# Kernel optimization log

Hardware: AMD Instinct MI355X
Metric: run time of the kernel (lower is better)

Reference implementation:

```python
import jax, jax.numpy as jnp
import numpy as np

B, S, D, H, DH = 2, 2048, 768, 12, 64
GAMMA = 0.5
SMOOTHING = 1.0  # softmax_attn_smoothing scalar (non-trainable weight in the original)
SCALE = 1.0 / float(np.sqrt(DH))


def setup_inputs() -> dict:
    key = jax.random.key(0)
    ks = jax.random.split(key, 8)
    w = 0.02
    return {
        "inp": jax.random.normal(ks[0], (B, S, D), dtype=jnp.float32),
        "pos_emb": jax.random.normal(ks[1], (S, D), dtype=jnp.float32),
        "Wq_inp": jax.random.normal(ks[2], (D, H * DH), dtype=jnp.float32) * w,
        "Wk_inp": jax.random.normal(ks[3], (D, H * DH), dtype=jnp.float32) * w,
        "Wq_pos": jax.random.normal(ks[4], (D, H * DH), dtype=jnp.float32) * w,
        "Wk_pos": jax.random.normal(ks[5], (D, H * DH), dtype=jnp.float32) * w,
        "Wv": jax.random.normal(ks[6], (D, H * DH), dtype=jnp.float32) * w,
        "Wo": jax.random.normal(ks[7], (H * DH, D), dtype=jnp.float32) * w,
    }


def reference(inp, pos_emb, Wq_inp, Wk_inp, Wq_pos, Wk_pos, Wv, Wo):
    # projections; note original reshape order: [..., d_head, n_head]
    q_i = (inp @ Wq_inp).reshape(B, S, DH, H)
    k_i = (inp @ Wk_inp).reshape(B, S, DH, H)
    q_p = (pos_emb @ Wq_pos).reshape(S, DH, H)
    k_p = (pos_emb @ Wk_pos).reshape(S, DH, H)
    v = (inp @ Wv).reshape(B, S, DH, H)

    # content-content stream: [B,S,S,H], softmax over key axis (axis=2)
    score_inp = jnp.einsum("bidh,bjdh->bijh", q_i, k_i) * (SCALE * SMOOTHING)
    prob_inp = jax.nn.softmax(score_inp, axis=2)

    # position-position stream: [S,S,H], softmax over key axis (axis=1)
    score_pos = jnp.einsum("idh,jdh->ijh", q_p, k_p) * (SCALE * SMOOTHING)
    prob_pos = jax.nn.softmax(score_pos, axis=1)[None]  # [1,S,S,H]

    # gamma blend of the two attention distributions
    attn_prob = (1.0 - GAMMA) * prob_inp + GAMMA * prob_pos  # [B,S,S,H]

    # V-weighted sum, merge heads as [..., h, d] per the original 'bihd' output
    attn_out = jnp.einsum("bijh,bjdh->bihd", attn_prob, v).reshape(B, S, H * DH)
    attn_out = attn_out @ Wo  # [B,S,D]
    return attn_out, attn_prob
```

## Files before the change

kernel.cpp:

```cpp
#include <hip/hip_runtime.h>
#include <hip/hip_bf16.h>

constexpr int NH  = 12;
constexpr int SEQ = 2048;
constexpr int DHD = 64;
constexpr int DIM = 768;
constexpr float QSCALE = 0.125f * 1.44269504088896f;

typedef __bf16 bf16x8 __attribute__((ext_vector_type(8)));
typedef __bf16 bf16x4 __attribute__((ext_vector_type(4)));
typedef float  f32x4  __attribute__((ext_vector_type(4)));

#define MFMA16(a, b, c) __builtin_amdgcn_mfma_f32_16x16x32_bf16((a), (b), (c), 0, 0, 0)

__global__ __launch_bounds__(256) void conv_kernel(
    const float* __restrict__ inp, const float* __restrict__ pos,
    __bf16* __restrict__ Ab, __bf16* __restrict__ Pb)
{
    const int idx = blockIdx.x * 256 + threadIdx.x;
    constexpr int N8I = 4096 * 768 / 8;
    constexpr int N8P = 2048 * 768 / 8;
    if (idx >= N8I + N8P) return;
    const float* src; __bf16* dst; int off;
    if (idx < N8I) { src = inp; dst = Ab; off = idx; }
    else           { src = pos; dst = Pb; off = idx - N8I; }
    const float4 v0 = *reinterpret_cast<const float4*>(&src[(size_t)off * 8]);
    const float4 v1 = *reinterpret_cast<const float4*>(&src[(size_t)off * 8 + 4]);
    bf16x8 t;
    t[0] = (__bf16)v0.x; t[1] = (__bf16)v0.y; t[2] = (__bf16)v0.z; t[3] = (__bf16)v0.w;
    t[4] = (__bf16)v1.x; t[5] = (__bf16)v1.y; t[6] = (__bf16)v1.z; t[7] = (__bf16)v1.w;
    *reinterpret_cast<bf16x8*>(&dst[(size_t)off * 8]) = t;
}

__global__ __launch_bounds__(256) void packw_kernel(
    const float* __restrict__ Wqi, const float* __restrict__ Wki,
    const float* __restrict__ Wvv, const float* __restrict__ Wqp,
    const float* __restrict__ Wkp, __bf16* __restrict__ Wp)
{
    const int kt = blockIdx.x, h = blockIdx.y, z = blockIdx.z;
    const int k0 = kt * 64;
    const float* W; float scale = 1.0f;
    if (z == 0)      { W = Wqi; scale = QSCALE; }
    else if (z == 1) { W = Wki; }
    else if (z == 2) { W = Wvv; }
    else if (z == 3) { W = Wqp; scale = QSCALE; }
    else             { W = Wkp; }

    __shared__ __bf16 lds[64][68];
    const int tid = threadIdx.x;
    {
        const int d = tid & 63, kq = tid >> 6;
        #pragma unroll
        for (int rep = 0; rep < 16; ++rep) {
            const int kk = rep * 4 + kq;
            lds[kk][d] = (__bf16)(W[(size_t)(k0 + kk) * DIM + d * 12 + h] * scale);
        }
    }
    __syncthreads();
    {
        const int k = tid & 63, dq = tid >> 6;
        const size_t slab = ((size_t)z * 12 + h) * 64;
        #pragma unroll
        for (int rep = 0; rep < 16; ++rep) {
            const int d = rep * 4 + dq;
            Wp[(slab + d) * DIM + k0 + k] = lds[k][d];
        }
    }
}

__global__ __launch_bounds__(256) void proj_kernel(
    const __bf16* __restrict__ Ab, const __bf16* __restrict__ Pb,
    const __bf16* __restrict__ Wp,
    __bf16* __restrict__ Qi, __bf16* __restrict__ Ki, __bf16* __restrict__ Vsd,
    __bf16* __restrict__ Qp, __bf16* __restrict__ Kp)
{
    const int bx = blockIdx.x, h = blockIdx.y, z = blockIdx.z;
    if (z >= 3 && bx >= 8) return;
    const int tid = threadIdx.x, lane = tid & 63, wv = tid >> 6;
    const int l15 = lane & 15, lg = lane >> 4;
    const int m_w = bx * 256 + wv * 64;

    const __bf16* Asrc = (z < 3) ? Ab : Pb;
    const __bf16* Wsl = Wp + ((size_t)z * 12 + h) * 64 * DIM;

    f32x4 acc[4][4] = {};

    for (int kt = 0; kt < 24; ++kt) {
        const int k0 = kt * 32;
        bf16x8 a[4], b[4];
        #pragma unroll
        for (int mf = 0; mf < 4; ++mf)
            a[mf] = *reinterpret_cast<const bf16x8*>(
                &Asrc[(size_t)(m_w + mf * 16 + l15) * DIM + k0 + lg * 8]);
        #pragma unroll
        for (int nf = 0; nf < 4; ++nf)
            b[nf] = *reinterpret_cast<const bf16x8*>(
                &Wsl[(size_t)(nf * 16 + l15) * DIM + k0 + lg * 8]);
        #pragma unroll
        for (int mf = 0; mf < 4; ++mf)
            #pragma unroll
            for (int nf = 0; nf < 4; ++nf)
                acc[mf][nf] = MFMA16(a[mf], b[nf], acc[mf][nf]);
    }

    __bf16* outp = (z == 0) ? Qi : (z == 1) ? Ki : (z == 2) ? Vsd : (z == 3) ? Qp : Kp;
    #pragma unroll
    for (int mf = 0; mf < 4; ++mf)
        #pragma unroll
        for (int r = 0; r < 4; ++r) {
            const int m = m_w + mf * 16 + lg * 4 + r;
            const int s = m & 2047;
            const int slab = (z < 3) ? ((m >> 11) * 12 + h) : h;
            const size_t base = ((size_t)slab * SEQ + s) * DHD;
            #pragma unroll
            for (int nf = 0; nf < 4; ++nf)
                outp[base + nf * 16 + l15] = (__bf16)acc[mf][nf][r];
        }
}

__global__ __launch_bounds__(256) void vtrans_kernel(
    const __bf16* __restrict__ Vsd, __bf16* __restrict__ Vt)
{
    const int s0 = blockIdx.x * 64, slab = blockIdx.y;
    __shared__ __bf16 lds[64][66];
    const int tid = threadIdx.x;
    {
        const int rr = tid >> 3, cq = tid & 7;
        #pragma unroll
        for (int rep = 0; rep < 2; ++rep) {
            const int r2 = rr + rep * 32;
            *reinterpret_cast<bf16x8*>(&lds[r2][cq * 8]) =
                *reinterpret_cast<const bf16x8*>(
                    &Vsd[((size_t)slab * SEQ + s0 + r2) * DHD + cq * 8]);
        }
    }
    __syncthreads();
    {
        const int dd = tid >> 3, sq = tid & 7;
        #pragma unroll
        for (int rep = 0; rep < 2; ++rep) {
            const int d2 = dd + rep * 32;
            bf16x8 v;
            #pragma unroll
            for (int q = 0; q < 8; ++q) v[q] = lds[sq * 8 + q][d2];
            *reinterpret_cast<bf16x8*>(&Vt[((size_t)slab * DHD + d2) * SEQ + s0 + sq * 8]) = v;
        }
    }
}

__global__ __launch_bounds__(64) void stats_kernel(
    const __bf16* __restrict__ Qi, const __bf16* __restrict__ Ki,
    const __bf16* __restrict__ Qp, const __bf16* __restrict__ Kp,
    float* __restrict__ m_ws, float* __restrict__ l_ws)
{
    const int bx = blockIdx.x, h = blockIdx.y, bb = blockIdx.z;
    const int lane = threadIdx.x;
    const int l15 = lane & 15, lg = lane >> 4;
    const int i0 = bx * 16;

    const __bf16* Q = (bb < 2) ? Qi + ((size_t)bb * NH + h) * SEQ * DHD
                               : Qp + (size_t)h * SEQ * DHD;
    const __bf16* K = (bb < 2) ? Ki + ((size_t)bb * NH + h) * SEQ * DHD
                               : Kp + (size_t)h * SEQ * DHD;

    bf16x8 a[2];
    #pragma unroll
    for (int ks = 0; ks < 2; ++ks)
        a[ks] = *reinterpret_cast<const bf16x8*>(
            &Q[(size_t)(i0 + l15) * DHD + ks * 32 + lg * 8]);

    float mr[4], lr[4];
    #pragma unroll
    for (int r = 0; r < 4; ++r) { mr[r] = -1e30f; lr[r] = 0.0f; }

    for (int jt = 0; jt < 32; ++jt) {
        const int j0 = jt * 64;
        bf16x8 bk[2][4];
        #pragma unroll
        for (int ks = 0; ks < 2; ++ks)
            #pragma unroll
            for (int nf = 0; nf < 4; ++nf)
                bk[ks][nf] = *reinterpret_cast<const bf16x8*>(
                    &K[(size_t)(j0 + nf * 16 + l15) * DHD + ks * 32 + lg * 8]);
        f32x4 c[4] = {};
        #pragma unroll
        for (int ks = 0; ks < 2; ++ks)
            #pragma unroll
            for (int nf = 0; nf < 4; ++nf)
                c[nf] = MFMA16(a[ks], bk[ks][nf], c[nf]);

        #pragma unroll
        for (int r = 0; r < 4; ++r) {
            const float x01 = fmaxf(c[0][r], c[1][r]);
            const float x23 = fmaxf(c[2][r], c[3][r]);
            const float mn = fmaxf(mr[r], fmaxf(x01, x23));
            lr[r] = lr[r] * exp2f(mr[r] - mn)
                  + exp2f(c[0][r] - mn) + exp2f(c[1][r] - mn)
                  + exp2f(c[2][r] - mn) + exp2f(c[3][r] - mn);
            mr[r] = mn;
        }
    }

    #pragma unroll
    for (int msk = 1; msk < 16; msk <<= 1)
        #pragma unroll
        for (int r = 0; r < 4; ++r) {
            const float mo = __shfl_xor(mr[r], msk);
            const float lo = __shfl_xor(lr[r], msk);
            const float mn = fmaxf(mr[r], mo);
            lr[r] = lr[r] * exp2f(mr[r] - mn) + lo * exp2f(mo - mn);
            mr[r] = mn;
        }

    if (l15 == 0) {
        const size_t base = ((size_t)bb * NH + h) * SEQ + i0;
        #pragma unroll
        for (int r = 0; r < 4; ++r) {
            m_ws[base + lg * 4 + r] = mr[r];
            l_ws[base + lg * 4 + r] = lr[r];
        }
    }
}

__global__ __launch_bounds__(384) void emit_kernel(
    const __bf16* __restrict__ Qi, const __bf16* __restrict__ Ki,
    const __bf16* __restrict__ Qp, const __bf16* __restrict__ Kp,
    const __bf16* __restrict__ Vt,
    const float* __restrict__ m_ws, const float* __restrict__ l_ws,
    float* __restrict__ out1, float* __restrict__ attn_pre)
{
    const int it = blockIdx.x, js = blockIdx.y, b = blockIdx.z;
    const int i0 = it * 16;
    const int tid = threadIdx.x, lane = tid & 63, wv = tid >> 6;
    const int l15 = lane & 15, lg = lane >> 4;

    __shared__ __align__(16) __bf16 pbuf[2][12][16][40];
    __shared__ float ml[12][16][4];

    if (tid < 192) {
        const int h = tid >> 4, i = tid & 15;
        const size_t bi  = ((size_t)b * NH + h) * SEQ + i0 + i;
        const size_t ppi = ((size_t)2 * NH + h) * SEQ + i0 + i;
        ml[h][i][0] = m_ws[bi];
        ml[h][i][1] = 0.5f / l_ws[bi];
        ml[h][i][2] = m_ws[ppi];
        ml[h][i][3] = 0.5f / l_ws[ppi];
    }
    __syncthreads();

    const __bf16* Kb[2][2];
    bf16x8 aQ[2][2][2];
    #pragma unroll
    for (int hh = 0; hh < 2; ++hh) {
        const int h = wv * 2 + hh;
        Kb[hh][0] = Ki + ((size_t)b * NH + h) * SEQ * DHD;
        Kb[hh][1] = Kp + (size_t)h * SEQ * DHD;
        #pragma unroll
        for (int ks = 0; ks < 2; ++ks) {
            aQ[hh][0][ks] = *reinterpret_cast<const bf16x8*>(
                &Qi[(((size_t)b * NH + h) * SEQ + i0 + l15) * DHD + ks * 32 + lg * 8]);
            aQ[hh][1][ks] = *reinterpret_cast<const bf16x8*>(
                &Qp[((size_t)h * SEQ + i0 + l15) * DHD + ks * 32 + lg * 8]);
        }
    }

    bf16x8 kf[2][2][2][2];
    {
        const int j0 = js * 256;
        #pragma unroll
        for (int hh = 0; hh < 2; ++hh)
            #pragma unroll
            for (int st = 0; st < 2; ++st)
                #pragma unroll
                for (int nf = 0; nf < 2; ++nf)
                    #pragma unroll
                    for (int ks = 0; ks < 2; ++ks)
                        kf[hh][st][nf][ks] = *reinterpret_cast<const bf16x8*>(
                            &Kb[hh][st][(size_t)(j0 + nf * 16 + l15) * DHD + ks * 32 + lg * 8]);
    }

    f32x4 acc[2][4] = {};

    #pragma unroll 1
    for (int jt = 0; jt < 8; ++jt) {
        const int j0 = js * 256 + jt * 32;
        const int jn = (js * 256 + (jt + 1) * 32) & (SEQ - 1);
        const int buf = jt & 1;

        f32x4 ci[2][2] = {}, cq[2][2] = {};
        #pragma unroll
        for (int hh = 0; hh < 2; ++hh)
            #pragma unroll
            for (int ks = 0; ks < 2; ++ks)
                #pragma unroll
                for (int nf = 0; nf < 2; ++nf) {
                    ci[hh][nf] = MFMA16(aQ[hh][0][ks], kf[hh][0][nf][ks], ci[hh][nf]);
                    cq[hh][nf] = MFMA16(aQ[hh][1][ks], kf[hh][1][nf][ks], cq[hh][nf]);
                }

        #pragma unroll
        for (int hh = 0; hh < 2; ++hh)
            #pragma unroll
            for (int st = 0; st < 2; ++st)
                #pragma unroll
                for (int nf = 0; nf < 2; ++nf)
                    #pragma unroll
                    for (int ks = 0; ks < 2; ++ks)
                        kf[hh][st][nf][ks] = *reinterpret_cast<const bf16x8*>(
                            &Kb[hh][st][(size_t)(jn + nf * 16 + l15) * DHD + ks * 32 + lg * 8]);

        #pragma unroll
        for (int hh = 0; hh < 2; ++hh) {
            const int h = wv * 2 + hh;
            #pragma unroll
            for (int r = 0; r < 4; ++r) {
                const int i = lg * 4 + r;
                const f32x4 mlv = *reinterpret_cast<const f32x4*>(&ml[h][i][0]);
                #pragma unroll
                for (int nf = 0; nf < 2; ++nf) {
                    const float pi_ = exp2f(ci[hh][nf][r] - mlv[0]) * mlv[1];
                    const float pq_ = exp2f(cq[hh][nf][r] - mlv[2]) * mlv[3];
                    pbuf[buf][h][i][nf * 16 + l15] = (__bf16)(pi_ + pq_);
                }
            }
        }

        #pragma unroll
        for (int hh = 0; hh < 2; ++hh) {
            const int h = wv * 2 + hh;
            const bf16x8 ap = *reinterpret_cast<const bf16x8*>(&pbuf[buf][h][l15][lg * 8]);
            #pragma unroll
            for (int nf = 0; nf < 4; ++nf) {
                const bf16x8 bv = *reinterpret_cast<const bf16x8*>(
                    &Vt[(((size_t)b * NH + h) * DHD + nf * 16 + l15) * SEQ + j0 + lg * 8]);
                acc[hh][nf] = MFMA16(ap, bv, acc[hh][nf]);
            }
        }
        __syncthreads();

        for (int p = tid; p < 512; p += 384) {
            const int i = p >> 5, jj = p & 31;
            const size_t base = (((size_t)(b * SEQ + i0 + i)) * SEQ + j0 + jj) * 12;
            f32x4 v0, v1, v2;
            #pragma unroll
            for (int q = 0; q < 4; ++q) {
                v0[q] = (float)pbuf[buf][q][i][jj];
                v1[q] = (float)pbuf[buf][4 + q][i][jj];
                v2[q] = (float)pbuf[buf][8 + q][i][jj];
            }
            *reinterpret_cast<f32x4*>(&out1[base])     = v0;
            *reinterpret_cast<f32x4*>(&out1[base + 4]) = v1;
            *reinterpret_cast<f32x4*>(&out1[base + 8]) = v2;
        }
    }

    #pragma unroll
    for (int hh = 0; hh < 2; ++hh) {
        const int h = wv * 2 + hh;
        #pragma unroll
        for (int nf = 0; nf < 4; ++nf)
            #pragma unroll
            for (int r = 0; r < 4; ++r) {
                const int i = lg * 4 + r;
                atomicAdd(&attn_pre[((size_t)(b * SEQ + i0 + i)) * DIM + h * DHD + nf * 16 + l15],
                          acc[hh][nf][r]);
            }
    }
}

__global__ __launch_bounds__(256) void final_kernel(
    const float* __restrict__ A, const float* __restrict__ W, float* __restrict__ out0)
{
    const int m0 = blockIdx.y * 64;
    const int n0 = blockIdx.x * 192;

    __shared__ __bf16 Al[64][32];
    __shared__ __bf16 Wl[192][32];

    const int tid = threadIdx.x;
    const int lane = tid & 63, wv = tid >> 6;
    const int wm = wv >> 1, wn = wv & 1;
    const int l15 = lane & 15, lg = lane >> 4;

    f32x4 c[2][6] = {};

    for (int kt = 0; kt < 24; ++kt) {
        const int k0 = kt * 32;
        __syncthreads();
        {
            const int r = tid >> 3, kq = tid & 7;
            #pragma unroll
            for (int rep = 0; rep < 2; ++rep) {
                const float4 v = *reinterpret_cast<const float4*>(
                    &A[(size_t)(m0 + r + rep * 32) * DIM + k0 + kq * 4]);
                bf16x4 t;
                t[0] = (__bf16)v.x; t[1] = (__bf16)v.y; t[2] = (__bf16)v.z; t[3] = (__bf16)v.w;
                *reinterpret_cast<bf16x4*>(&Al[r + rep * 32][kq * 4]) = t;
            }
        }
        for (int idx = tid; idx < 32 * 48; idx += 256) {
            const int k = idx / 48, nq = idx - k * 48;
            const float4 v = *reinterpret_cast<const float4*>(
                &W[(size_t)(k0 + k) * DIM + n0 + nq * 4]);
            Wl[nq * 4 + 0][k] = (__bf16)v.x;
            Wl[nq * 4 + 1][k] = (__bf16)v.y;
            Wl[nq * 4 + 2][k] = (__bf16)v.z;
            Wl[nq * 4 + 3][k] = (__bf16)v.w;
        }
        __syncthreads();

        bf16x8 a[2], b[6];
        #pragma unroll
        for (int mf = 0; mf < 2; ++mf)
            a[mf] = *reinterpret_cast<const bf16x8*>(&Al[wm * 32 + mf * 16 + l15][lg * 8]);
        #pragma unroll
        for (int nf = 0; nf < 6; ++nf)
            b[nf] = *reinterpret_cast<const bf16x8*>(&Wl[wn * 96 + nf * 16 + l15][lg * 8]);
        #pragma unroll
        for (int mf = 0; mf < 2; ++mf)
            #pragma unroll
            for (int nf = 0; nf < 6; ++nf)
                c[mf][nf] = MFMA16(a[mf], b[nf], c[mf][nf]);
    }

    #pragma unroll
    for (int mf = 0; mf < 2; ++mf)
        #pragma unroll
        for (int nf = 0; nf < 6; ++nf)
            #pragma unroll
            for (int r = 0; r < 4; ++r) {
                const int m = m0 + wm * 32 + mf * 16 + lg * 4 + r;
                const int n = n0 + wn * 96 + nf * 16 + l15;
                out0[(size_t)m * DIM + n] = c[mf][nf][r];
            }
}

extern "C" void kernel_launch(void* const* d_in, const int* in_sizes, int n_in,
                              void* d_out, int out_size, void* d_ws, size_t ws_size,
                              hipStream_t stream)
{
    (void)in_sizes; (void)n_in; (void)out_size; (void)ws_size;

    const float* inp = (const float*)d_in[0];
    const float* pos = (const float*)d_in[1];
    const float* Wqi = (const float*)d_in[2];
    const float* Wki = (const float*)d_in[3];
    const float* Wqp = (const float*)d_in[4];
    const float* Wkp = (const float*)d_in[5];
    const float* Wvv = (const float*)d_in[6];
    const float* Wo  = (const float*)d_in[7];

    char* w = (char*)d_ws;
    __bf16* Ab = (__bf16*)w;  w += (size_t)4096 * 768 * 2;
    __bf16* Pb = (__bf16*)w;  w += (size_t)2048 * 768 * 2;
    __bf16* Wp = (__bf16*)w;  w += (size_t)5 * 768 * 768 * 2;
    __bf16* Qi = (__bf16*)w;  w += (size_t)2 * NH * SEQ * DHD * 2;
    __bf16* Ki = (__bf16*)w;  w += (size_t)2 * NH * SEQ * DHD * 2;
    __bf16* Vsd = (__bf16*)w; w += (size_t)2 * NH * SEQ * DHD * 2;
    __bf16* Qp = (__bf16*)w;  w += (size_t)NH * SEQ * DHD * 2;
    __bf16* Kp = (__bf16*)w;  w += (size_t)NH * SEQ * DHD * 2;
    float* m_ws = (float*)w;  w += (size_t)3 * NH * SEQ * 4;
    float* l_ws = (float*)w;  w += (size_t)3 * NH * SEQ * 4;
    float* attn_pre = (float*)w; w += (size_t)4096 * DIM * 4;
    __bf16* Vt = Ab;

    float* out0 = (float*)d_out;
    float* out1 = out0 + (size_t)2 * SEQ * DIM;

    hipMemsetAsync(attn_pre, 0, (size_t)4096 * DIM * 4, stream);

    hipLaunchKernelGGL(conv_kernel, dim3(2304), dim3(256), 0, stream, inp, pos, Ab, Pb);
    hipLaunchKernelGGL(packw_kernel, dim3(12, 12, 5), dim3(256), 0, stream,
                       Wqi, Wki, Wvv, Wqp, Wkp, Wp);
    hipLaunchKernelGGL(proj_kernel, dim3(16, 12, 5), dim3(256), 0, stream,
                       Ab, Pb, Wp, Qi, Ki, Vsd, Qp, Kp);
    hipLaunchKernelGGL(vtrans_kernel, dim3(32, 24), dim3(256), 0, stream, Vsd, Vt);
    hipLaunchKernelGGL(stats_kernel, dim3(128, 12, 3), dim3(64), 0, stream,
                       Qi, Ki, Qp, Kp, m_ws, l_ws);
    hipLaunchKernelGGL(emit_kernel, dim3(128, 8, 2), dim3(384), 0, stream,
                       Qi, Ki, Qp, Kp, Vt, m_ws, l_ws, out1, attn_pre);
    hipLaunchKernelGGL(final_kernel, dim3(4, 64, 1), dim3(256), 0, stream,
                       attn_pre, Wo, out0);
}
```

Before: 734.1 us.

## Retile projection per head, remap block order, widen emit key span, stage attn_prob store

```diff
diff --git a/kernel.cpp b/kernel.cpp
--- a/kernel.cpp
+++ b/kernel.cpp
@@ -74,48 +74,42 @@
     __bf16* __restrict__ Qi, __bf16* __restrict__ Ki, __bf16* __restrict__ Vsd,
     __bf16* __restrict__ Qp, __bf16* __restrict__ Kp)
 {
-    const int bx = blockIdx.x, h = blockIdx.y, z = blockIdx.z;
-    if (z >= 3 && bx >= 8) return;
+    const int bx = blockIdx.x, z = blockIdx.y;
+    if (z >= 3 && bx >= 32) return;
     const int tid = threadIdx.x, lane = tid & 63, wv = tid >> 6;
     const int l15 = lane & 15, lg = lane >> 4;
-    const int m_w = bx * 256 + wv * 64;
+    const int m_w = bx * 64 + wv * 16;
 
     const __bf16* Asrc = (z < 3) ? Ab : Pb;
-    const __bf16* Wsl = Wp + ((size_t)z * 12 + h) * 64 * DIM;
-
-    f32x4 acc[4][4] = {};
-
-    for (int kt = 0; kt < 24; ++kt) {
-        const int k0 = kt * 32;
-        bf16x8 a[4], b[4];
-        #pragma unroll
-        for (int mf = 0; mf < 4; ++mf)
-            a[mf] = *reinterpret_cast<const bf16x8*>(
-                &Asrc[(size_t)(m_w + mf * 16 + l15) * DIM + k0 + lg * 8]);
-        #pragma unroll
-        for (int nf = 0; nf < 4; ++nf)
-            b[nf] = *reinterpret_cast<const bf16x8*>(
-                &Wsl[(size_t)(nf * 16 + l15) * DIM + k0 + lg * 8]);
-        #pragma unroll
-        for (int mf = 0; mf < 4; ++mf)
+    __bf16* outp = (z == 0) ? Qi : (z == 1) ? Ki : (z == 2) ? Vsd : (z == 3) ? Qp : Kp;
+    const int slab_b = (z < 3) ? ((m_w >> 11) * 12) : 0;
+    const int s_base = m_w & 2047;
+
+    for (int h = 0; h < 12; ++h) {
+        const __bf16* Wsl = Wp + ((size_t)z * 12 + h) * 64 * DIM;
+        f32x4 acc[4] = {};
+        for (int kt = 0; kt < 24; ++kt) {
+            const int k0 = kt * 32;
+            const bf16x8 a = *reinterpret_cast<const bf16x8*>(
+                &Asrc[(size_t)(m_w + l15) * DIM + k0 + lg * 8]);
+            bf16x8 bfr[4];
             #pragma unroll
             for (int nf = 0; nf < 4; ++nf)
-                acc[mf][nf] = MFMA16(a[mf], b[nf], acc[mf][nf]);
-    }
-
-    __bf16* outp = (z == 0) ? Qi : (z == 1) ? Ki : (z == 2) ? Vsd : (z == 3) ? Qp : Kp;
-    #pragma unroll
-    for (int mf = 0; mf < 4; ++mf)
+                bfr[nf] = *reinterpret_cast<const bf16x8*>(
+                    &Wsl[(size_t)(nf * 16 + l15) * DIM + k0 + lg * 8]);
+            #pragma unroll
+            for (int nf = 0; nf < 4; ++nf)
+                acc[nf] = MFMA16(a, bfr[nf], acc[nf]);
+        }
+        const size_t base = ((size_t)(slab_b + h) * SEQ + s_base);
         #pragma unroll
         for (int r = 0; r < 4; ++r) {
-            const int m = m_w + mf * 16 + lg * 4 + r;
-            const int s = m & 2047;
-            const int slab = (z < 3) ? ((m >> 11) * 12 + h) : h;
-            const size_t base = ((size_t)slab * SEQ + s) * DHD;
+            const size_t rowb = (base + lg * 4 + r) * DHD;
             #pragma unroll
             for (int nf = 0; nf < 4; ++nf)
-                outp[base + nf * 16 + l15] = (__bf16)acc[mf][nf][r];
-        }
+                outp[rowb + nf * 16 + l15] = (__bf16)acc[nf][r];
+        }
+    }
 }
 
 __global__ __launch_bounds__(256) void vtrans_kernel(
@@ -153,7 +147,10 @@
     const __bf16* __restrict__ Qp, const __bf16* __restrict__ Kp,
     float* __restrict__ m_ws, float* __restrict__ l_ws)
 {
-    const int bx = blockIdx.x, h = blockIdx.y, bb = blockIdx.z;
+    const int bid = blockIdx.x + 128 * (blockIdx.y + 12 * blockIdx.z);
+    const int wg = (bid & 7) * 576 + (bid >> 3);
+    const int bx = wg & 127, h = (wg >> 7) % 12, bb = wg / 1536;
+
     const int lane = threadIdx.x;
     const int l15 = lane & 15, lg = lane >> 4;
     const int i0 = bx * 16;
@@ -229,13 +226,18 @@
     const float* __restrict__ m_ws, const float* __restrict__ l_ws,
     float* __restrict__ out1, float* __restrict__ attn_pre)
 {
-    const int it = blockIdx.x, js = blockIdx.y, b = blockIdx.z;
+    const int bid = blockIdx.x + 128 * (blockIdx.y + 4 * blockIdx.z);
+    const int wg = (bid & 7) * 128 + (bid >> 3);
+    const int it = wg & 127, js = (wg >> 7) & 3, b = wg >> 9;
+
     const int i0 = it * 16;
     const int tid = threadIdx.x, lane = tid & 63, wv = tid >> 6;
     const int l15 = lane & 15, lg = lane >> 4;
 
-    __shared__ __align__(16) __bf16 pbuf[2][12][16][40];
+    __shared__ __align__(16) __bf16 ppv[12][16][40];
+    __shared__ __align__(16) __bf16 pb2[2][16][32][12];
     __shared__ float ml[12][16][4];
+    const __bf16* p2flat = &pb2[0][0][0][0];
 
     if (tid < 192) {
         const int h = tid >> 4, i = tid & 15;
@@ -266,7 +268,7 @@
 
     bf16x8 kf[2][2][2][2];
     {
-        const int j0 = js * 256;
+        const int j0 = js * 512;
         #pragma unroll
         for (int hh = 0; hh < 2; ++hh)
             #pragma unroll
@@ -282,9 +284,9 @@
     f32x4 acc[2][4] = {};
 
     #pragma unroll 1
-    for (int jt = 0; jt < 8; ++jt) {
-        const int j0 = js * 256 + jt * 32;
-        const int jn = (js * 256 + (jt + 1) * 32) & (SEQ - 1);
+    for (int jt = 0; jt < 16; ++jt) {
+        const int j0 = js * 512 + jt * 32;
+        const int jn = (js * 512 + (jt + 1) * 32) & (SEQ - 1);
         const int buf = jt & 1;
 
         f32x4 ci[2][2] = {}, cq[2][2] = {};
@@ -320,7 +322,10 @@
                 for (int nf = 0; nf < 2; ++nf) {
                     const float pi_ = exp2f(ci[hh][nf][r] - mlv[0]) * mlv[1];
                     const float pq_ = exp2f(cq[hh][nf][r] - mlv[2]) * mlv[3];
-                    pbuf[buf][h][i][nf * 16 + l15] = (__bf16)(pi_ + pq_);
+                    const __bf16 p = (__bf16)(pi_ + pq_);
+                    const int jj = nf * 16 + l15;
+                    ppv[h][i][jj] = p;
+                    pb2[buf][i][jj][h] = p;
                 }
             }
         }
@@ -328,7 +333,7 @@
         #pragma unroll
         for (int hh = 0; hh < 2; ++hh) {
             const int h = wv * 2 + hh;
-            const bf16x8 ap = *reinterpret_cast<const bf16x8*>(&pbuf[buf][h][l15][lg * 8]);
+            const bf16x8 ap = *reinterpret_cast<const bf16x8*>(&ppv[h][l15][lg * 8]);
             #pragma unroll
             for (int nf = 0; nf < 4; ++nf) {
                 const bf16x8 bv = *reinterpret_cast<const bf16x8*>(
@@ -338,19 +343,17 @@
         }
         __syncthreads();
 
-        for (int p = tid; p < 512; p += 384) {
-            const int i = p >> 5, jj = p & 31;
-            const size_t base = (((size_t)(b * SEQ + i0 + i)) * SEQ + j0 + jj) * 12;
-            f32x4 v0, v1, v2;
-            #pragma unroll
-            for (int q = 0; q < 4; ++q) {
-                v0[q] = (float)pbuf[buf][q][i][jj];
-                v1[q] = (float)pbuf[buf][4 + q][i][jj];
-                v2[q] = (float)pbuf[buf][8 + q][i][jj];
-            }
-            *reinterpret_cast<f32x4*>(&out1[base])     = v0;
-            *reinterpret_cast<f32x4*>(&out1[base + 4]) = v1;
-            *reinterpret_cast<f32x4*>(&out1[base + 8]) = v2;
+        #pragma unroll
+        for (int k = 0; k < 4; ++k) {
+            const int o = (wv * 4 + k) * 256 + 4 * lane;
+            const int i = o / 384;
+            const int rem = o - i * 384;
+            const bf16x4 pv4 = *reinterpret_cast<const bf16x4*>(&p2flat[buf * 6144 + o]);
+            f32x4 v;
+            #pragma unroll
+            for (int q = 0; q < 4; ++q) v[q] = (float)pv4[q];
+            const size_t addr = ((size_t)(b * SEQ + i0 + i) * SEQ + j0) * 12 + rem;
+            *reinterpret_cast<f32x4*>(&out1[addr]) = v;
         }
     }
 
@@ -472,12 +475,12 @@
     hipLaunchKernelGGL(conv_kernel, dim3(2304), dim3(256), 0, stream, inp, pos, Ab, Pb);
     hipLaunchKernelGGL(packw_kernel, dim3(12, 12, 5), dim3(256), 0, stream,
                        Wqi, Wki, Wvv, Wqp, Wkp, Wp);
-    hipLaunchKernelGGL(proj_kernel, dim3(16, 12, 5), dim3(256), 0, stream,
+    hipLaunchKernelGGL(proj_kernel, dim3(64, 5), dim3(256), 0, stream,
                        Ab, Pb, Wp, Qi, Ki, Vsd, Qp, Kp);
     hipLaunchKernelGGL(vtrans_kernel, dim3(32, 24), dim3(256), 0, stream, Vsd, Vt);
     hipLaunchKernelGGL(stats_kernel, dim3(128, 12, 3), dim3(64), 0, stream,
                        Qi, Ki, Qp, Kp, m_ws, l_ws);
-    hipLaunchKernelGGL(emit_kernel, dim3(128, 8, 2), dim3(384), 0, stream,
+    hipLaunchKernelGGL(emit_kernel, dim3(128, 4, 2), dim3(384), 0, stream,
                        Qi, Ki, Qp, Kp, Vt, m_ws, l_ws, out1, attn_pre);
     hipLaunchKernelGGL(final_kernel, dim3(4, 64, 1), dim3(256), 0, stream,
                        attn_pre, Wo, out0);
```

Measured after the change: 943.1 us. 28.5% more time.
